# Kernel tuning notes

Hardware: AMD Instinct MI355X
Metric: run time of the kernel (lower is better)

The kernel has to match this reference:

```python
import jax, jax.numpy as jnp
import numpy as np

N_NODES = 100000
N_EDGES = 3200000
IN_DIM = 128
HID_DIM = 64
OUT_DIM = 2
N_GRAPHS = 512


def setup_inputs() -> dict:
    key = jax.random.key(0)
    ks = jax.random.split(key, 8)
    x = jax.random.normal(ks[0], (N_NODES, IN_DIM), dtype=jnp.float32)
    edge_index = jax.random.randint(ks[1], (2, N_EDGES), 0, N_NODES, dtype=jnp.int64)
    batch = jnp.sort(jax.random.randint(ks[2], (N_NODES,), 0, N_GRAPHS, dtype=jnp.int64))
    # GCNConv params (glorot-ish scale)
    W_gcn = jax.random.normal(ks[3], (IN_DIM, HID_DIM), dtype=jnp.float32) / np.sqrt(IN_DIM)
    b_gcn = jnp.zeros((HID_DIM,), dtype=jnp.float32)
    # MLP params: Linear(hid,hid) -> ReLU -> Linear(hid,out)
    W1 = jax.random.normal(ks[4], (HID_DIM, HID_DIM), dtype=jnp.float32) / np.sqrt(HID_DIM)
    b1 = jnp.zeros((HID_DIM,), dtype=jnp.float32)
    W2 = jax.random.normal(ks[5], (HID_DIM, OUT_DIM), dtype=jnp.float32) / np.sqrt(HID_DIM)
    b2 = jnp.zeros((OUT_DIM,), dtype=jnp.float32)
    return {"x": x, "edge_index": edge_index, "batch": batch,
            "W_gcn": W_gcn, "b_gcn": b_gcn, "W1": W1, "b1": b1, "W2": W2, "b2": b2}


def reference(x, edge_index, batch, W_gcn, b_gcn, W1, b1, W2, b2):
    n = x.shape[0]
    # --- GCNConv: add self-loops, symmetric normalization, aggregate, transform ---
    self_loop = jnp.arange(n, dtype=edge_index.dtype)
    row = jnp.concatenate([edge_index[0], self_loop])  # source nodes
    col = jnp.concatenate([edge_index[1], self_loop])  # target nodes
    deg = jax.ops.segment_sum(jnp.ones_like(col, dtype=x.dtype), col, num_segments=n)
    dinv = jnp.where(deg > 0, jax.lax.rsqrt(deg), 0.0)
    norm = dinv[row] * dinv[col]                       # (E+N,)
    xw = x @ W_gcn                                     # (N, hid) transform first (in_dim > hid)
    msg = xw[row] * norm[:, None]                      # gather + scale
    z = jax.ops.segment_sum(msg, col, num_segments=n) + b_gcn  # scatter-add
    z = jax.nn.relu(z)
    # --- global mean pool over graphs ---
    sums = jax.ops.segment_sum(z, batch, num_segments=N_GRAPHS)          # (G, hid)
    cnts = jax.ops.segment_sum(jnp.ones((n,), z.dtype), batch, num_segments=N_GRAPHS)
    g = sums / jnp.maximum(cnts, 1.0)[:, None]
    # --- MLP -> sigmoid ---
    h = jax.nn.relu(g @ W1 + b1)
    return jax.nn.sigmoid(h @ W2 + b2)                 # (G, out_dim)
```

## Files before the change

kernel.cpp:

```cpp
#include <hip/hip_runtime.h>

#define N_NODES 100000
#define N_EDGES 3200000
#define IN_DIM 128
#define HID_DIM 64
#define OUT_DIM 2
#define N_GRAPHS 512

#define BSHIFT 6
#define NBK 1563
#define NBB 512
#define EPB3 6250
#define CAPSHIFT 12
#define LDS_E2 2816
#define ZERO_ROW N_NODES

__device__ inline unsigned short f2bf(float f) {
    union { float f; unsigned int i; } v; v.f = f;
    unsigned int r = v.i + 0x7fffu + ((v.i >> 16) & 1u);
    return (unsigned short)(r >> 16);
}

typedef __attribute__((ext_vector_type(8))) short bf16x8;
typedef __attribute__((ext_vector_type(4))) float f32x4;
typedef __attribute__((ext_vector_type(2))) float f32x2;

__global__ __launch_bounds__(1024) void k_init(float* __restrict__ gsum,
                                               int* __restrict__ cnt_g,
                                               float* __restrict__ gcnt,
                                               unsigned char* __restrict__ xws) {
    int b = blockIdx.x, t = threadIdx.x;
    if (b < 32) {
        gsum[b * 1024 + t] = 0.f;
    } else if (b < 34) {
        int j = (b - 32) * 1024 + t;
        if (j < NBK) cnt_g[j] = 0;
    } else {
        if (t < N_GRAPHS) gcnt[t] = 0.f;
        if (t >= 1008)
            ((int*)(xws + (size_t)ZERO_ROW * HID_DIM))[t - 1008] = 0;
    }
}

__global__ __launch_bounds__(512) void k_bin(const int* __restrict__ row,
                                             const int* __restrict__ col,
                                             int* __restrict__ cnt_g,
                                             int* __restrict__ binned) {
    __shared__ int h[NBK];
    __shared__ int lofs[NBK];
    __shared__ int cur[NBK];
    __shared__ int ps[512];
    __shared__ int sorted[EPB3];
    __shared__ unsigned short bkt16[EPB3];
    int t = threadIdx.x;
    for (int i = t; i < NBK; i += 512) { h[i] = 0; cur[i] = 0; }
    __syncthreads();
    int s = blockIdx.x * EPB3, e = s + EPB3;
    for (int i = s + t; i < e; i += 512)
        atomicAdd(&h[col[i] >> BSHIFT], 1);
    __syncthreads();
    {
        int b0 = t << 2;
        int loc[4];
        int run = 0;
#pragma unroll
        for (int j = 0; j < 4; j++) {
            int b = b0 + j;
            loc[j] = run;
            run += (b < NBK) ? h[b] : 0;
        }
        ps[t] = run;
        __syncthreads();
        for (int off = 1; off < 512; off <<= 1) {
            int v = (t >= off) ? ps[t - off] : 0;
            __syncthreads();
            ps[t] += v;
            __syncthreads();
        }
        int base = (t > 0) ? ps[t - 1] : 0;
#pragma unroll
        for (int j = 0; j < 4; j++) {
            int b = b0 + j;
            if (b < NBK) lofs[b] = base + loc[j];
        }
    }
    __syncthreads();
    for (int i = t; i < NBK; i += 512) {
        int hv = h[i];
        if (hv) h[i] = (i << CAPSHIFT) + atomicAdd(&cnt_g[i], hv);
    }
    __syncthreads();
    for (int i = s + t; i < e; i += 512) {
        int c = col[i];
        int r = row[i];
        int bk = c >> BSHIFT;
        int rk = atomicAdd(&cur[bk], 1);
        int p = lofs[bk] + rk;
        sorted[p] = ((c & 63) << 17) | r;
        bkt16[p] = (unsigned short)bk;
    }
    __syncthreads();
    for (int i = t; i < EPB3; i += 512) {
        int bk = bkt16[i];
        binned[h[bk] + (i - lofs[bk])] = sorted[i];
    }
}

__global__ __launch_bounds__(256) void k_gemm(const float* __restrict__ x,
                                              const float* __restrict__ Wg,
                                              const int* __restrict__ cnt_g,
                                              const int* __restrict__ binned,
                                              int* __restrict__ degs,
                                              unsigned char* __restrict__ xws) {
    __shared__ unsigned short wb[16][64][8];
    __shared__ int cnt[64];

    if (threadIdx.x < 64) cnt[threadIdx.x] = 0;
    for (int idx = threadIdx.x; idx < 1024; idx += 256) {
        int f = idx >> 6, l = idx & 63;
        int ks = f >> 2, nt = f & 3;
        int n = (l & 15) + (nt << 4);
        int kbase = (ks << 5) + ((l >> 4) << 3);
        unsigned short tmp[8];
#pragma unroll
        for (int j = 0; j < 8; j++)
            tmp[j] = f2bf(Wg[(kbase + j) * HID_DIM + n]);
        *(bf16x8*)&wb[f][l][0] = *(const bf16x8*)tmp;
    }
    __syncthreads();

    int bkt = blockIdx.x;
    int m = cnt_g[bkt];
    for (int i = threadIdx.x; i < m; i += 256)
        atomicAdd(&cnt[binned[(bkt << CAPSHIFT) + i] >> 17], 1);

    int wave = threadIdx.x >> 6;
    int lane = threadIdx.x & 63;
    int q = lane >> 4, nn = lane & 15;

    bf16x8 bfrag[4][4];
#pragma unroll
    for (int ks = 0; ks < 4; ks++)
#pragma unroll
        for (int nt = 0; nt < 4; nt++)
            bfrag[ks][nt] = *(const bf16x8*)&wb[ks * 4 + nt][lane][0];

    int node0 = bkt * 64 + wave * 16;
    int arow = node0 + nn;
    if (arow > N_NODES - 1) arow = N_NODES - 1;
    const float* xrow = x + (size_t)arow * IN_DIM + (q << 3);

    f32x4 acc[4] = {{0.f,0.f,0.f,0.f},{0.f,0.f,0.f,0.f},
                    {0.f,0.f,0.f,0.f},{0.f,0.f,0.f,0.f}};
#pragma unroll
    for (int ks = 0; ks < 4; ks++) {
        float4 xa = *(const float4*)(xrow + ks * 32);
        float4 xb_ = *(const float4*)(xrow + ks * 32 + 4);
        bf16x8 af;
        af[0] = (short)f2bf(xa.x); af[1] = (short)f2bf(xa.y);
        af[2] = (short)f2bf(xa.z); af[3] = (short)f2bf(xa.w);
        af[4] = (short)f2bf(xb_.x); af[5] = (short)f2bf(xb_.y);
        af[6] = (short)f2bf(xb_.z); af[7] = (short)f2bf(xb_.w);
#pragma unroll
        for (int nt = 0; nt < 4; nt++)
            acc[nt] = __builtin_amdgcn_mfma_f32_16x16x32_bf16(af, bfrag[ks][nt], acc[nt], 0, 0, 0);
    }
    __syncthreads();

    if (threadIdx.x < 64) degs[bkt * 64 + threadIdx.x] = cnt[threadIdx.x];

#pragma unroll
    for (int r = 0; r < 4; r++) {
        int lrow = wave * 16 + q * 4 + r;
        int mrow = bkt * 64 + lrow;
        if (mrow < N_NODES) {
            float dn = rsqrtf((float)cnt[lrow] + 1.0f);
            int p01 = __builtin_amdgcn_cvt_pk_fp8_f32(acc[0][r] * dn, acc[1][r] * dn, 0, false);
            int p23 = __builtin_amdgcn_cvt_pk_fp8_f32(acc[2][r] * dn, acc[3][r] * dn, 0, false);
            unsigned char* rp = xws + (size_t)mrow * HID_DIM + nn;
            rp[0]  = (unsigned char)(p01 & 0xff);
            rp[16] = (unsigned char)((p01 >> 8) & 0xff);
            rp[32] = (unsigned char)(p23 & 0xff);
            rp[48] = (unsigned char)((p23 >> 8) & 0xff);
        }
    }
}

__global__ __launch_bounds__(512) void k_aggrf(const unsigned char* __restrict__ xws,
                                               const int* __restrict__ binned,
                                               const int* __restrict__ cnt_g,
                                               const int* __restrict__ degs,
                                               const int* __restrict__ batch,
                                               const float* __restrict__ bg,
                                               float* __restrict__ gsum,
                                               float* __restrict__ gcnt) {
    int bkt = blockIdx.x;
    int nbase = bkt << BSHIFT;
    int nnodes = N_NODES - nbase; if (nnodes > 64) nnodes = 64;
    int m = cnt_g[bkt];
    int base = bkt << CAPSHIFT;

    __shared__ int cnt[64];
    __shared__ int lptr[65];
    __shared__ int cur[64];
    __shared__ int sb[64];
    __shared__ float gcl[8];
    __shared__ alignas(16) int srt[LDS_E2];
    __shared__ float pool[8][4][64];

    if (threadIdx.x < 64) {
        int n = nbase + threadIdx.x;
        cnt[threadIdx.x] = (threadIdx.x < nnodes) ? degs[bkt * 64 + threadIdx.x] : 0;
        sb[threadIdx.x]  = (threadIdx.x < nnodes) ? batch[n] : 0;
        cur[threadIdx.x] = 0;
    }
    if (threadIdx.x < 8) gcl[threadIdx.x] = 0.f;
    for (int t = threadIdx.x; t < 8 * 4 * 64; t += 512)
        ((float*)pool)[t] = 0.f;
    __syncthreads();

    if (threadIdx.x < 64) {
        int v = (threadIdx.x < nnodes) ? ((cnt[threadIdx.x] + 8) & ~7) : 0;
        int run = v;
#pragma unroll
        for (int off = 1; off < 64; off <<= 1) {
            int t = __shfl_up(run, off);
            if (threadIdx.x >= off) run += t;
        }
        lptr[threadIdx.x + 1] = run;
        if (threadIdx.x == 0) lptr[0] = 0;
    }
    __syncthreads();
    int tot = lptr[64]; if (tot > LDS_E2) tot = LDS_E2;
    for (int i = threadIdx.x; i < tot; i += 512) srt[i] = ZERO_ROW << 6;
    __syncthreads();
    if (threadIdx.x < nnodes) {
        int p = lptr[threadIdx.x] + cnt[threadIdx.x];
        if (p < LDS_E2) srt[p] = (nbase + threadIdx.x) << 6;
        int sl = sb[threadIdx.x] - sb[0];
        if (sl < 8) atomicAdd(&gcl[sl], 1.0f);
        else atomicAdd(&gcnt[sb[threadIdx.x]], 1.0f);
    }
    for (int i = threadIdx.x; i < m; i += 512) {
        int pk = binned[base + i];
        int nid = pk >> 17;
        int rk = atomicAdd(&cur[nid], 1);
        int pos = lptr[nid] + rk;
        if (pos < LDS_E2) srt[pos] = (pk & 0x1FFFF) << 6;
    }
    __syncthreads();

    int wave = threadIdx.x >> 6;
    int lane = threadIdx.x & 63;
    int sub = lane >> 4;
    int lc  = lane & 15;
    int l4  = lc << 2;
    const unsigned char* xbl = xws + l4;
    int g0 = sb[0];
    float4 bia = ((const float4*)bg)[lc];

#pragma unroll
    for (int r = 0; r < 2; r++) {
        int ln = wave * 8 + sub * 2 + r;
        int valid = (ln < nnodes);
        int s0 = valid ? lptr[ln] : 0;
        int e0 = valid ? lptr[ln + 1] : 0;
        if (s0 > LDS_E2) s0 = LDS_E2;
        if (e0 > LDS_E2) e0 = LDS_E2;
        f32x2 al0 = {0.f,0.f}, ah0 = {0.f,0.f};
        f32x2 al1 = {0.f,0.f}, ah1 = {0.f,0.f};
        for (int i = s0; i < e0; i += 8) {
            int4 ra = *(const int4*)&srt[i];
            int4 rb = *(const int4*)&srt[i + 4];
            unsigned int d0 = *(const unsigned int*)(xbl + ra.x);
            unsigned int d1 = *(const unsigned int*)(xbl + ra.y);
            unsigned int d2 = *(const unsigned int*)(xbl + ra.z);
            unsigned int d3 = *(const unsigned int*)(xbl + ra.w);
            unsigned int d4 = *(const unsigned int*)(xbl + rb.x);
            unsigned int d5 = *(const unsigned int*)(xbl + rb.y);
            unsigned int d6 = *(const unsigned int*)(xbl + rb.z);
            unsigned int d7 = *(const unsigned int*)(xbl + rb.w);
            f32x2 p;
            p = __builtin_amdgcn_cvt_pk_f32_fp8(d0, false); al0 += p;
            p = __builtin_amdgcn_cvt_pk_f32_fp8(d0, true);  ah0 += p;
            p = __builtin_amdgcn_cvt_pk_f32_fp8(d1, false); al1 += p;
            p = __builtin_amdgcn_cvt_pk_f32_fp8(d1, true);  ah1 += p;
            p = __builtin_amdgcn_cvt_pk_f32_fp8(d2, false); al0 += p;
            p = __builtin_amdgcn_cvt_pk_f32_fp8(d2, true);  ah0 += p;
            p = __builtin_amdgcn_cvt_pk_f32_fp8(d3, false); al1 += p;
            p = __builtin_amdgcn_cvt_pk_f32_fp8(d3, true);  ah1 += p;
            p = __builtin_amdgcn_cvt_pk_f32_fp8(d4, false); al0 += p;
            p = __builtin_amdgcn_cvt_pk_f32_fp8(d4, true);  ah0 += p;
            p = __builtin_amdgcn_cvt_pk_f32_fp8(d5, false); al1 += p;
            p = __builtin_amdgcn_cvt_pk_f32_fp8(d5, true);  ah1 += p;
            p = __builtin_amdgcn_cvt_pk_f32_fp8(d6, false); al0 += p;
            p = __builtin_amdgcn_cvt_pk_f32_fp8(d6, true);  ah0 += p;
            p = __builtin_amdgcn_cvt_pk_f32_fp8(d7, false); al1 += p;
            p = __builtin_amdgcn_cvt_pk_f32_fp8(d7, true);  ah1 += p;
        }
        f32x2 alo = al0 + al1, ahi = ah0 + ah1;
        int slot = 99;
        float4 val;
        if (valid) {
            float dn = rsqrtf((float)cnt[ln] + 1.0f);
            val.x = fmaxf(alo[0] * dn + bia.x, 0.f);
            val.y = fmaxf(alo[1] * dn + bia.y, 0.f);
            val.z = fmaxf(ahi[0] * dn + bia.z, 0.f);
            val.w = fmaxf(ahi[1] * dn + bia.w, 0.f);
            slot = sb[ln] - g0;
        }
#pragma unroll
        for (int ss = 0; ss < 4; ss++) {
            if (sub == ss && slot < 4) {
                float4* pp = (float4*)&pool[wave][slot][l4];
                float4 pv = *pp;
                pv.x += val.x; pv.y += val.y; pv.z += val.z; pv.w += val.w;
                *pp = pv;
            }
        }
        if (slot >= 4 && slot < 99) {
            float* gp = &gsum[sb[ln] * HID_DIM + l4];
            atomicAdd(gp + 0, val.x); atomicAdd(gp + 1, val.y);
            atomicAdd(gp + 2, val.z); atomicAdd(gp + 3, val.w);
        }
    }
    __syncthreads();

    if (threadIdx.x < 8) {
        float c = gcl[threadIdx.x];
        if (c != 0.f) atomicAdd(&gcnt[g0 + threadIdx.x], c);
    }
    for (int t = threadIdx.x; t < 4 * 64; t += 512) {
        int slot = t >> 6, j = t & 63;
        float v = 0.f;
#pragma unroll
        for (int w2 = 0; w2 < 8; w2++) v += pool[w2][slot][j];
        if (v != 0.f) atomicAdd(&gsum[(g0 + slot) * HID_DIM + j], v);
    }
}

__global__ __launch_bounds__(64) void k_mlp(const float* __restrict__ gsum,
                                            const float* __restrict__ gcnt,
                                            const float* __restrict__ W1,
                                            const float* __restrict__ b1,
                                            const float* __restrict__ W2,
                                            const float* __restrict__ b2,
                                            float* __restrict__ out) {
    int g = blockIdx.x;
    int j = threadIdx.x;
    float cnt = fmaxf(gcnt[g], 1.0f);

    __shared__ float gs[64];
    __shared__ float hs[64];
    gs[j] = gsum[g * 64 + j] / cnt;
    __syncthreads();

    float h = b1[j];
    for (int k = 0; k < 64; k++) h += gs[k] * W1[k * 64 + j];
    hs[j] = fmaxf(h, 0.f);
    __syncthreads();

    if (j < OUT_DIM) {
        float o = b2[j];
        for (int k = 0; k < 64; k++) o += hs[k] * W2[k * OUT_DIM + j];
        out[g * OUT_DIM + j] = 1.f / (1.f + expf(-o));
    }
}

extern "C" void kernel_launch(void* const* d_in, const int* in_sizes, int n_in,
                              void* d_out, int out_size, void* d_ws, size_t ws_size,
                              hipStream_t stream) {
    const float* x   = (const float*)d_in[0];
    const int* eidx  = (const int*)d_in[1];
    const int* batch = (const int*)d_in[2];
    const float* Wg  = (const float*)d_in[3];
    const float* bg  = (const float*)d_in[4];
    const float* W1  = (const float*)d_in[5];
    const float* b1  = (const float*)d_in[6];
    const float* W2  = (const float*)d_in[7];
    const float* b2  = (const float*)d_in[8];
    float* out = (float*)d_out;

    char* w = (char*)d_ws;
    unsigned char* xws = (unsigned char*)w;     w += (size_t)(N_NODES + 1) * HID_DIM;
    int*   binned  = (int*)w;                   w += ((size_t)NBK << CAPSHIFT) * 4;
    int*   cnt_g   = (int*)w;                   w += NBK * 4;
    int*   degs    = (int*)w;                   w += (size_t)NBK * 64 * 4;
    float* gsum    = (float*)w;                 w += N_GRAPHS * HID_DIM * 4;
    float* gcnt    = (float*)w;                 w += N_GRAPHS * 4;

    const int* rowp = eidx;
    const int* colp = eidx + N_EDGES;

    k_init<<<35, 1024, 0, stream>>>(gsum, cnt_g, gcnt, xws);
    k_bin<<<NBB, 512, 0, stream>>>(rowp, colp, cnt_g, binned);
    k_gemm<<<NBK, 256, 0, stream>>>(x, Wg, cnt_g, binned, degs, xws);
    k_aggrf<<<NBK, 512, 0, stream>>>(xws, binned, cnt_g, degs, batch, bg, gsum, gcnt);
    k_mlp<<<N_GRAPHS, 64, 0, stream>>>(gsum, gcnt, W1, b1, W2, b2, out);
}
```

Measured before the change: 192.0 us.

## Shard bucket counters into 8 sub-slots and shrink binning blocks

The binning kernel now runs twice as many blocks, each handling half as many edges. Each bucket's global counter is split into 8 sub-counters, each owning a 512-entry sub-range of the bucket, which spreads the global atomic contention. The LDS staging now holds only a 16-bit edge index instead of the packed value plus bucket id, so col and row are re-read from global memory in sorted order. The downstream kernels scan all 4096 slots per bucket and skip entries beyond each sub-count, which adds some strided loop overhead. Capacity is now 512 per sub-slot, so a skewed input could overflow.

```diff
diff --git a/kernel.cpp b/kernel.cpp
--- a/kernel.cpp
+++ b/kernel.cpp
@@ -9,9 +9,10 @@
 
 #define BSHIFT 6
 #define NBK 1563
-#define NBB 512
-#define EPB3 6250
+#define NBB 1024
+#define EPB2 3125
 #define CAPSHIFT 12
+#define SUBSHIFT 9
 #define LDS_E2 2816
 #define ZERO_ROW N_NODES
 
@@ -32,9 +33,9 @@
     int b = blockIdx.x, t = threadIdx.x;
     if (b < 32) {
         gsum[b * 1024 + t] = 0.f;
-    } else if (b < 34) {
+    } else if (b < 45) {
         int j = (b - 32) * 1024 + t;
-        if (j < NBK) cnt_g[j] = 0;
+        if (j < NBK * 8) cnt_g[j] = 0;
     } else {
         if (t < N_GRAPHS) gcnt[t] = 0.f;
         if (t >= 1008)
@@ -50,14 +51,13 @@
     __shared__ int lofs[NBK];
     __shared__ int cur[NBK];
     __shared__ int ps[512];
-    __shared__ int sorted[EPB3];
-    __shared__ unsigned short bkt16[EPB3];
+    __shared__ unsigned short idx16[EPB2];
     int t = threadIdx.x;
     for (int i = t; i < NBK; i += 512) { h[i] = 0; cur[i] = 0; }
     __syncthreads();
-    int s = blockIdx.x * EPB3, e = s + EPB3;
-    for (int i = s + t; i < e; i += 512)
-        atomicAdd(&h[col[i] >> BSHIFT], 1);
+    int s = blockIdx.x * EPB2;
+    for (int i = t; i < EPB2; i += 512)
+        atomicAdd(&h[col[s + i] >> BSHIFT], 1);
     __syncthreads();
     {
         int b0 = t << 2;
@@ -85,24 +85,25 @@
         }
     }
     __syncthreads();
+    int xs = blockIdx.x & 7;
     for (int i = t; i < NBK; i += 512) {
         int hv = h[i];
-        if (hv) h[i] = (i << CAPSHIFT) + atomicAdd(&cnt_g[i], hv);
-    }
-    __syncthreads();
-    for (int i = s + t; i < e; i += 512) {
-        int c = col[i];
-        int r = row[i];
+        if (hv) h[i] = (i << CAPSHIFT) + (xs << SUBSHIFT)
+                     + atomicAdd(&cnt_g[(i << 3) + xs], hv);
+    }
+    __syncthreads();
+    for (int i = t; i < EPB2; i += 512) {
+        int bk = col[s + i] >> BSHIFT;
+        int rk = atomicAdd(&cur[bk], 1);
+        idx16[lofs[bk] + rk] = (unsigned short)i;
+    }
+    __syncthreads();
+    for (int i = t; i < EPB2; i += 512) {
+        int idx = idx16[i];
+        int c = col[s + idx];
+        int r = row[s + idx];
         int bk = c >> BSHIFT;
-        int rk = atomicAdd(&cur[bk], 1);
-        int p = lofs[bk] + rk;
-        sorted[p] = ((c & 63) << 17) | r;
-        bkt16[p] = (unsigned short)bk;
-    }
-    __syncthreads();
-    for (int i = t; i < EPB3; i += 512) {
-        int bk = bkt16[i];
-        binned[h[bk] + (i - lofs[bk])] = sorted[i];
+        binned[h[bk] + (i - lofs[bk])] = ((c & 63) << 17) | r;
     }
 }
 
@@ -114,8 +115,11 @@
                                               unsigned char* __restrict__ xws) {
     __shared__ unsigned short wb[16][64][8];
     __shared__ int cnt[64];
-
+    __shared__ int cnt8[8];
+
+    int bkt = blockIdx.x;
     if (threadIdx.x < 64) cnt[threadIdx.x] = 0;
+    if (threadIdx.x < 8) cnt8[threadIdx.x] = cnt_g[(bkt << 3) + threadIdx.x];
     for (int idx = threadIdx.x; idx < 1024; idx += 256) {
         int f = idx >> 6, l = idx & 63;
         int ks = f >> 2, nt = f & 3;
@@ -129,10 +133,9 @@
     }
     __syncthreads();
 
-    int bkt = blockIdx.x;
-    int m = cnt_g[bkt];
-    for (int i = threadIdx.x; i < m; i += 256)
-        atomicAdd(&cnt[binned[(bkt << CAPSHIFT) + i] >> 17], 1);
+    for (int i = threadIdx.x; i < (1 << CAPSHIFT); i += 256)
+        if ((i & ((1 << SUBSHIFT) - 1)) < cnt8[i >> SUBSHIFT])
+            atomicAdd(&cnt[binned[(bkt << CAPSHIFT) + i] >> 17], 1);
 
     int wave = threadIdx.x >> 6;
     int lane = threadIdx.x & 63;
@@ -197,13 +200,13 @@
     int bkt = blockIdx.x;
     int nbase = bkt << BSHIFT;
     int nnodes = N_NODES - nbase; if (nnodes > 64) nnodes = 64;
-    int m = cnt_g[bkt];
     int base = bkt << CAPSHIFT;
 
     __shared__ int cnt[64];
     __shared__ int lptr[65];
     __shared__ int cur[64];
     __shared__ int sb[64];
+    __shared__ int cnt8[8];
     __shared__ float gcl[8];
     __shared__ alignas(16) int srt[LDS_E2];
     __shared__ float pool[8][4][64];
@@ -214,7 +217,10 @@
         sb[threadIdx.x]  = (threadIdx.x < nnodes) ? batch[n] : 0;
         cur[threadIdx.x] = 0;
     }
-    if (threadIdx.x < 8) gcl[threadIdx.x] = 0.f;
+    if (threadIdx.x < 8) {
+        gcl[threadIdx.x] = 0.f;
+        cnt8[threadIdx.x] = cnt_g[(bkt << 3) + threadIdx.x];
+    }
     for (int t = threadIdx.x; t < 8 * 4 * 64; t += 512)
         ((float*)pool)[t] = 0.f;
     __syncthreads();
@@ -241,12 +247,14 @@
         if (sl < 8) atomicAdd(&gcl[sl], 1.0f);
         else atomicAdd(&gcnt[sb[threadIdx.x]], 1.0f);
     }
-    for (int i = threadIdx.x; i < m; i += 512) {
-        int pk = binned[base + i];
-        int nid = pk >> 17;
-        int rk = atomicAdd(&cur[nid], 1);
-        int pos = lptr[nid] + rk;
-        if (pos < LDS_E2) srt[pos] = (pk & 0x1FFFF) << 6;
+    for (int i = threadIdx.x; i < (1 << CAPSHIFT); i += 512) {
+        if ((i & ((1 << SUBSHIFT) - 1)) < cnt8[i >> SUBSHIFT]) {
+            int pk = binned[base + i];
+            int nid = pk >> 17;
+            int rk = atomicAdd(&cur[nid], 1);
+            int pos = lptr[nid] + rk;
+            if (pos < LDS_E2) srt[pos] = (pk & 0x1FFFF) << 6;
+        }
     }
     __syncthreads();
 
@@ -384,7 +392,7 @@
     char* w = (char*)d_ws;
     unsigned char* xws = (unsigned char*)w;     w += (size_t)(N_NODES + 1) * HID_DIM;
     int*   binned  = (int*)w;                   w += ((size_t)NBK << CAPSHIFT) * 4;
-    int*   cnt_g   = (int*)w;                   w += NBK * 4;
+    int*   cnt_g   = (int*)w;                   w += (size_t)NBK * 8 * 4;
     int*   degs    = (int*)w;                   w += (size_t)NBK * 64 * 4;
     float* gsum    = (float*)w;                 w += N_GRAPHS * HID_DIM * 4;
     float* gcnt    = (float*)w;                 w += N_GRAPHS * 4;
@@ -392,7 +400,7 @@
     const int* rowp = eidx;
     const int* colp = eidx + N_EDGES;
 
-    k_init<<<35, 1024, 0, stream>>>(gsum, cnt_g, gcnt, xws);
+    k_init<<<46, 1024, 0, stream>>>(gsum, cnt_g, gcnt, xws);
     k_bin<<<NBB, 512, 0, stream>>>(rowp, colp, cnt_g, binned);
     k_gemm<<<NBK, 256, 0, stream>>>(x, Wg, cnt_g, binned, degs, xws);
     k_aggrf<<<NBK, 512, 0, stream>>>(xws, binned, cnt_g, degs, batch, bg, gsum, gcnt);
```

After: 242.1 us. 26.1% more time.
